# Optimization experiments

Measured on AMD Instinct MI355X. Metric: run time of the kernel, lower is better.

Reference implementation:

```python
import jax, jax.numpy as jnp
import numpy as np
from jax import lax

DN = ('NCHW', 'OIHW', 'NCHW')
NUM_HEADS = 6


def _conv1x1(x, w):
    return lax.conv_general_dilated(x, w, (1, 1), 'VALID', dimension_numbers=DN)


def _dwconv3x3(x, w):
    # depthwise 3x3, groups == channels, padding 1
    return lax.conv_general_dilated(x, w, (1, 1), ((1, 1), (1, 1)),
                                    dimension_numbers=DN,
                                    feature_group_count=w.shape[0])


def setup_inputs() -> dict:
    key = jax.random.key(0)
    ks = jax.random.split(key, 7)
    b, dim, h, w = 4, 192, 128, 128
    inp = {
        'x': jax.random.normal(ks[0], (b, dim, h, w), jnp.float32),
        'ref': jax.random.normal(ks[1], (b, dim, h, w), jnp.float32),
        'w_qkv': jax.random.normal(ks[2], (dim * 3, dim, 1, 1), jnp.float32) * 0.05,
        'w_dw': jax.random.normal(ks[3], (dim * 3, 1, 3, 3), jnp.float32) * 0.1,
        'w_proj': jax.random.normal(ks[4], (dim, dim, 1, 1), jnp.float32) * 0.05,
        'temperature': jnp.ones((NUM_HEADS, 1, 1), jnp.float32),
        'attn_w': 0.2 * jnp.ones((4,), jnp.float32),
    }
    return inp


def reference(x, ref, w_qkv, w_dw, w_proj, temperature, attn_w):
    b, c, h, w = x.shape
    heads = NUM_HEADS
    C = c // heads  # per-head channel dim
    hw = h * w

    qkv = _dwconv3x3(_conv1x1(x, w_qkv), w_dw)        # [b, 3c, h, w]
    ref_qkv = _dwconv3x3(_conv1x1(ref, w_qkv), w_dw)  # shared weights

    q_shared = qkv[:, :c]            # q from x
    k_shared = ref_qkv[:, c:2 * c]   # k from ref
    v_shared = ref_qkv[:, 2 * c:]    # v from ref

    def to_heads(t):  # [b, c, h, w] -> [b, head, C, hw]
        return t.reshape(b, heads, C, hw)

    q = to_heads(q_shared)
    k = to_heads(k_shared)
    v = to_heads(v_shared)

    # L2-normalize along token dim (last axis)
    q = q / jnp.maximum(jnp.linalg.norm(q, axis=-1, keepdims=True), 1e-12)
    k = k / jnp.maximum(jnp.linalg.norm(k, axis=-1, keepdims=True), 1e-12)

    # channel-wise attention: [b, head, C, C]
    attn = jnp.einsum('bhcn,bhdn->bhcd', q, k) * temperature

    ks_list = [int(C / 2), int(C * 2 / 3), int(C * 3 / 4), int(C * 4 / 5)]
    neg_inf = jnp.asarray(-jnp.inf, attn.dtype)

    out = 0.0
    for i, ki in enumerate(ks_list):
        vals = lax.top_k(attn, ki)[0]            # [b, head, C, ki]
        thr = vals[..., -1:]                     # k-th largest per row
        a = jnp.where(attn >= thr, attn, neg_inf)
        a = jax.nn.softmax(a, axis=-1)
        out = out + attn_w[i] * jnp.einsum('bhcd,bhdn->bhcn', a, v)

    out = out.reshape(b, c, h, w)
    return _conv1x1(out, w_proj)
```

## Files before the change

kernel.cpp:

```cpp
#include <hip/hip_runtime.h>
#include <cstdint>
#include <cstddef>

typedef unsigned short u16;
typedef unsigned int u32;
typedef __attribute__((ext_vector_type(2))) float f32x2;
typedef __attribute__((ext_vector_type(4))) float f32x4;
typedef __attribute__((ext_vector_type(8))) short short8;
typedef __attribute__((ext_vector_type(2))) u32 u32x2;
typedef __attribute__((ext_vector_type(4))) u32 u32x4;

#define DEV static __device__ __forceinline__
#define HW 16384

DEV u16 f2bf(float f) {
  u32 u = __float_as_uint(f);
  u = (u + 0x7fffu + ((u >> 16) & 1u)) >> 16;
  return (u16)u;
}
DEV float bf2f(u16 h) { return __uint_as_float(((u32)h) << 16); }

DEV u32 packsplit(float f) {
  u16 h = f2bf(f);
  u16 l = f2bf(f - bf2f(h));
  return (u32)h | ((u32)l << 16);
}
DEV void unpack8(const u32* w, short8& hi, short8& lo) {
  #pragma unroll
  for (int i = 0; i < 8; ++i) {
    hi[i] = (short)(u16)w[i];
    lo[i] = (short)(u16)(w[i] >> 16);
  }
}
DEV void mfma3(f32x4& acc, short8 ah, short8 al, short8 bh, short8 bl) {
  acc = __builtin_amdgcn_mfma_f32_16x16x32_bf16(ah, bh, acc, 0, 0, 0);
  acc = __builtin_amdgcn_mfma_f32_16x16x32_bf16(ah, bl, acc, 0, 0, 0);
  acc = __builtin_amdgcn_mfma_f32_16x16x32_bf16(al, bh, acc, 0, 0, 0);
}

__global__ __launch_bounds__(256) void ksplit(const float* __restrict__ in,
                                              u32* __restrict__ out, int n) {
  int i = blockIdx.x * 256 + threadIdx.x;
  if (i < n) out[i] = packsplit(in[i]);
}

template<int ABATCH, int BPACKED>
__global__ __launch_bounds__(512, 4) void gemm6(const u32* __restrict__ Asp,
                                                const u32* __restrict__ B0,
                                                const u32* __restrict__ B1,
                                                float* __restrict__ C0,
                                                float* __restrict__ C1) {
  __shared__ u16 Ah[192 * 32];
  __shared__ u16 Al[192 * 32];
  __shared__ u32 Bs[128 * 34];
  const int t = threadIdx.x, lane = t & 63, wid = t >> 6;
  const int b = blockIdx.z, n0 = blockIdx.x * 128, y = blockIdx.y;
  const int m0 = y * 192;
  const u32* Ab = Asp + (ABATCH ? (size_t)b * 192 * 192 : 0) + (size_t)m0 * 192;
  const u32* Bb = (y == 0 ? B0 : B1) + (size_t)b * 192 * (size_t)HW;
  float* Cb = (y == 0) ? (C0 + (size_t)b * 192 * (size_t)HW)
                       : (C1 + ((size_t)b * 384 + (size_t)(y - 1) * 192) * (size_t)HW);
  const int wr = wid >> 2, wc = wid & 3;
  const int g = lane >> 4, r16 = lane & 15;
  const int bk = t >> 4;
  const int bn = t & 15;
  f32x4 acc[6][2] = {};

  int adst[3];
  int asrc_row[3], asrc_kc[3];
  #pragma unroll
  for (int i = 0; i < 3; ++i) {
    int vi = t + i * 512;
    int row = vi >> 3, kv = (vi & 7) << 2;
    asrc_row[i] = row; asrc_kc[i] = kv;
    adst[i] = row * 32 + (((kv >> 3) ^ ((row >> 1) & 3)) << 3) + (kv & 7);
  }
  const int aswz = (g ^ ((r16 >> 1) & 3)) << 3;

  u32 Breg[8], Bnext[8];
  u32x4 Areg[3];
  #pragma unroll
  for (int j = 0; j < 8; ++j)
    Breg[j] = Bb[(size_t)bk * HW + n0 + bn + 16 * j];
  #pragma unroll
  for (int i = 0; i < 3; ++i)
    Areg[i] = *(const u32x4*)&Ab[(size_t)asrc_row[i] * 192 + asrc_kc[i]];
  #pragma unroll 1
  for (int p = 0; p < 6; ++p) {
    #pragma unroll
    for (int j = 0; j < 8; ++j)
      Bs[(bn + 16 * j) * 34 + bk] =
          BPACKED ? Breg[j] : packsplit(__uint_as_float(Breg[j]));
    #pragma unroll
    for (int i = 0; i < 3; ++i) {
      u32 h01 = (Areg[i][0] & 0xffffu) | (Areg[i][1] << 16);
      u32 h23 = (Areg[i][2] & 0xffffu) | (Areg[i][3] << 16);
      u32 l01 = (Areg[i][0] >> 16) | (Areg[i][1] & 0xffff0000u);
      u32 l23 = (Areg[i][2] >> 16) | (Areg[i][3] & 0xffff0000u);
      u32x2 hq = {h01, h23}, lq = {l01, l23};
      *(u32x2*)&Ah[adst[i]] = hq;
      *(u32x2*)&Al[adst[i]] = lq;
    }
    if (p < 5) {
      #pragma unroll
      for (int j = 0; j < 8; ++j)
        Bnext[j] = Bb[(size_t)((p + 1) * 32 + bk) * HW + n0 + bn + 16 * j];
    }
    __syncthreads();
    if (p < 5) {
      #pragma unroll
      for (int i = 0; i < 3; ++i)
        Areg[i] = *(const u32x4*)&Ab[(size_t)asrc_row[i] * 192 + (p + 1) * 32 + asrc_kc[i]];
    }
    short8 bh[2], bl[2];
    #pragma unroll
    for (int nf = 0; nf < 2; ++nf) {
      u32 bw[8];
      const u32* bp = &Bs[(wc * 32 + nf * 16 + r16) * 34 + g * 8];
      *(u32x2*)&bw[0] = *(const u32x2*)&bp[0];
      *(u32x2*)&bw[2] = *(const u32x2*)&bp[2];
      *(u32x2*)&bw[4] = *(const u32x2*)&bp[4];
      *(u32x2*)&bw[6] = *(const u32x2*)&bp[6];
      unpack8(bw, bh[nf], bl[nf]);
    }
    #pragma unroll
    for (int mf = 0; mf < 6; ++mf) {
      const int ar = (wr * 96 + mf * 16 + r16) * 32 + aswz;
      short8 ah = *(const short8*)&Ah[ar];
      short8 al = *(const short8*)&Al[ar];
      #pragma unroll
      for (int nf = 0; nf < 2; ++nf) {
        acc[mf][nf] = __builtin_amdgcn_mfma_f32_16x16x32_bf16(ah, bh[nf], acc[mf][nf], 0, 0, 0);
        acc[mf][nf] = __builtin_amdgcn_mfma_f32_16x16x32_bf16(ah, bl[nf], acc[mf][nf], 0, 0, 0);
        acc[mf][nf] = __builtin_amdgcn_mfma_f32_16x16x32_bf16(al, bh[nf], acc[mf][nf], 0, 0, 0);
      }
    }
    __syncthreads();
    #pragma unroll
    for (int j = 0; j < 8; ++j) Breg[j] = Bnext[j];
  }
  #pragma unroll
  for (int mf = 0; mf < 6; ++mf)
    #pragma unroll
    for (int nf = 0; nf < 2; ++nf)
      #pragma unroll
      for (int rr = 0; rr < 4; ++rr)
        Cb[(size_t)(wr * 96 + mf * 16 + g * 4 + rr) * HW + n0 + wc * 32 + nf * 16 + r16] =
            acc[mf][nf][rr];
}

template<int SSQ>
__global__ __launch_bounds__(512) void k2_dw(const float* __restrict__ Tin, int cstIn,
                                             const float* __restrict__ wdw, int wco,
                                             u32* __restrict__ O,
                                             float* __restrict__ ssq, int sspath) {
  const int rt = blockIdx.x, cg = blockIdx.y, b = blockIdx.z;
  const int t = threadIdx.x, lane = t & 63, w = t >> 6;
  __shared__ float In[8][10][132];
  for (int idx = t; idx < 10400; idx += 512) {
    int ch = idx / 1300, rem = idx % 1300;
    int r = rem / 130, ci = rem % 130;
    int gr = rt * 8 + r - 1, gc = ci - 1;
    float v = 0.f;
    if (gr >= 0 && gr < 128 && gc >= 0 && gc < 128)
      v = Tin[((size_t)b * cstIn + cg * 8 + ch) * HW + gr * 128 + gc];
    In[ch][r][ci] = v;
  }
  float wv[9];
  #pragma unroll
  for (int j = 0; j < 9; ++j) wv[j] = wdw[(size_t)(wco + cg * 8 + w) * 9 + j];
  __syncthreads();
  float s = 0.f;
  u32* Op = O + ((size_t)b * 192 + cg * 8 + w) * HW + rt * 8 * 128 + 2 * lane;
  #pragma unroll
  for (int i = 0; i < 8; ++i) {
    float a0 = 0.f, a1 = 0.f;
    #pragma unroll
    for (int dr = 0; dr < 3; ++dr) {
      f32x2 u0 = *(const f32x2*)&In[w][i + dr][2 * lane];
      f32x2 u1 = *(const f32x2*)&In[w][i + dr][2 * lane + 2];
      a0 += wv[dr * 3] * u0[0] + wv[dr * 3 + 1] * u0[1] + wv[dr * 3 + 2] * u1[0];
      a1 += wv[dr * 3] * u0[1] + wv[dr * 3 + 1] * u1[0] + wv[dr * 3 + 2] * u1[1];
    }
    u32x2 o = {packsplit(a0), packsplit(a1)};
    *(u32x2*)&Op[(size_t)i * 128] = o;
    if (SSQ) s += a0 * a0 + a1 * a1;
  }
  if (SSQ) {
    #pragma unroll
    for (int off = 32; off; off >>= 1) s += __shfl_down(s, off);
    if (lane == 0) ssq[(((size_t)b * 2 + sspath) * 192 + cg * 8 + w) * 16 + rt] = s;
  }
}

__global__ __launch_bounds__(256) void k3_gram(const u32* __restrict__ q,
                                               const u32* __restrict__ k,
                                               float* __restrict__ gp) {
  const int ck = blockIdx.x, bh = blockIdx.y;
  const int b = bh / 6, h = bh % 6;
  const int t = threadIdx.x, lane = t & 63, wid = t >> 6;
  const int r16 = lane & 15, g = lane >> 4;
  const int chunk = ck * 4 + wid;
  const size_t rbase = ((size_t)b * 192 + h * 32 + r16) * HW;
  const u32* qp = q + rbase;
  const u32* kp = k + rbase;
  __shared__ float red[4][1024];
  f32x4 acc[2][2] = {};
  #pragma unroll 1
  for (int s = 0; s < 8; ++s) {
    int n = chunk * 256 + s * 32 + g * 8;
    u32 wq0[8], wq1[8], wk0[8], wk1[8];
    *(u32x4*)&wq0[0] = *(const u32x4*)&qp[n];
    *(u32x4*)&wq0[4] = *(const u32x4*)&qp[n + 4];
    *(u32x4*)&wq1[0] = *(const u32x4*)&qp[(size_t)16 * HW + n];
    *(u32x4*)&wq1[4] = *(const u32x4*)&qp[(size_t)16 * HW + n + 4];
    *(u32x4*)&wk0[0] = *(const u32x4*)&kp[n];
    *(u32x4*)&wk0[4] = *(const u32x4*)&kp[n + 4];
    *(u32x4*)&wk1[0] = *(const u32x4*)&kp[(size_t)16 * HW + n];
    *(u32x4*)&wk1[4] = *(const u32x4*)&kp[(size_t)16 * HW + n + 4];
    short8 a0h, a0l, a1h, a1l, b0h, b0l, b1h, b1l;
    unpack8(wq0, a0h, a0l);
    unpack8(wq1, a1h, a1l);
    unpack8(wk0, b0h, b0l);
    unpack8(wk1, b1h, b1l);
    mfma3(acc[0][0], a0h, a0l, b0h, b0l);
    mfma3(acc[0][1], a0h, a0l, b1h, b1l);
    mfma3(acc[1][0], a1h, a1l, b0h, b0l);
    mfma3(acc[1][1], a1h, a1l, b1h, b1l);
  }
  #pragma unroll
  for (int mf = 0; mf < 2; ++mf)
    #pragma unroll
    for (int nf = 0; nf < 2; ++nf)
      #pragma unroll
      for (int rr = 0; rr < 4; ++rr)
        red[wid][(mf * 16 + g * 4 + rr) * 32 + nf * 16 + r16] = acc[mf][nf][rr];
  __syncthreads();
  float* outp = gp + ((size_t)bh * 16 + ck) * 1024;
  #pragma unroll
  for (int e = t; e < 1024; e += 256)
    outp[e] = red[0][e] + red[1][e] + red[2][e] + red[3][e];
}

__global__ __launch_bounds__(512) void k4_comb(const float* __restrict__ gp,
                                               const float* __restrict__ ssq,
                                               const float* __restrict__ temp,
                                               const float* __restrict__ aw,
                                               const float* __restrict__ wproj,
                                               u32* __restrict__ mcp) {
  const int bh = blockIdx.x, b = bh / 6, h = bh % 6;
  const int t = threadIdx.x;
  __shared__ float Gs[1024];
  __shared__ float Acm[1024];
  __shared__ float Wp[192 * 32];
  __shared__ float nq[32], nk[32];
  #pragma unroll
  for (int i = 0; i < 3; ++i) {
    int idx = t + i * 512;
    int row = idx >> 3, c4 = (idx & 7) << 2;
    *(f32x4*)&Wp[row * 32 + c4] = *(const f32x4*)&wproj[(size_t)row * 192 + h * 32 + c4];
  }
  {
    const float* p = gp + (size_t)bh * 16 * 1024 + 2 * t;
    f32x2 s = {};
    #pragma unroll
    for (int ch = 0; ch < 16; ++ch) {
      f32x2 v = *(const f32x2*)&p[(size_t)ch * 1024];
      s[0] += v[0]; s[1] += v[1];
    }
    *(f32x2*)&Gs[2 * t] = s;
  }
  if (t < 64) {
    int c = t & 31, pk = t >> 5;
    const float* sp = ssq + (((size_t)b * 2 + pk) * 192 + h * 32 + c) * 16;
    f32x4 s4 = {};
    #pragma unroll
    for (int i = 0; i < 4; ++i) {
      f32x4 v = *(const f32x4*)&sp[4 * i];
      s4[0] += v[0]; s4[1] += v[1]; s4[2] += v[2]; s4[3] += v[3];
    }
    float nr = fmaxf(sqrtf(s4[0] + s4[1] + s4[2] + s4[3]), 1e-12f);
    if (pk == 0) nq[c] = nr; else nk[c] = nr;
  }
  __syncthreads();
  const float T = temp[h];
  {
    int c = (2 * t) >> 5;
    f32x2 v = *(const f32x2*)&Gs[2 * t];
    float inq = T / nq[c];
    v[0] = v[0] * inq / nk[(2 * t) & 31];
    v[1] = v[1] * inq / nk[(2 * t + 1) & 31];
    __syncthreads();
    *(f32x2*)&Gs[2 * t] = v;
  }
  __syncthreads();
  const float aw0 = aw[0], aw1 = aw[1], aw2 = aw[2], aw3 = aw[3];
  const int half = t >> 5, d = t & 31;
  #pragma unroll
  for (int it = 0; it < 2; ++it) {
    const int c = it * 16 + half;
    const float v = Gs[c * 32 + d];
    int cnt = 0;
    #pragma unroll
    for (int dd = 0; dd < 32; ++dd) cnt += (Gs[c * 32 + dd] >= v) ? 1 : 0;
    float c0 = v;
    float c1 = (cnt >= 16) ? v : -3.0e38f;
    float c2 = (cnt >= 21) ? v : -3.0e38f;
    float c3 = (cnt >= 24) ? v : -3.0e38f;
    float c4 = (cnt >= 25) ? v : -3.0e38f;
    #pragma unroll
    for (int off = 16; off; off >>= 1) {
      c0 = fmaxf(c0, __shfl_xor(c0, off));
      c1 = fmaxf(c1, __shfl_xor(c1, off));
      c2 = fmaxf(c2, __shfl_xor(c2, off));
      c3 = fmaxf(c3, __shfl_xor(c3, off));
      c4 = fmaxf(c4, __shfl_xor(c4, off));
    }
    const float m = c0;
    const float ex = expf(v - m);
    float z1 = (v >= c1) ? ex : 0.f;
    float z2 = (v >= c2) ? ex : 0.f;
    float z3 = (v >= c3) ? ex : 0.f;
    float z4 = (v >= c4) ? ex : 0.f;
    #pragma unroll
    for (int off = 16; off; off >>= 1) {
      z1 += __shfl_xor(z1, off);
      z2 += __shfl_xor(z2, off);
      z3 += __shfl_xor(z3, off);
      z4 += __shfl_xor(z4, off);
    }
    float a = 0.f;
    a += (v >= c1) ? aw0 * ex / z1 : 0.f;
    a += (v >= c2) ? aw1 * ex / z2 : 0.f;
    a += (v >= c3) ? aw2 * ex / z3 : 0.f;
    a += (v >= c4) ? aw3 * ex / z4 : 0.f;
    Acm[c * 32 + d] = a;
  }
  __syncthreads();
  #pragma unroll
  for (int i = 0; i < 12; ++i) {
    int idx = t + i * 512;
    int co = idx >> 5, dd = idx & 31;
    float s = 0.f;
    #pragma unroll
    for (int c = 0; c < 32; ++c) s += Wp[co * 32 + c] * Acm[c * 32 + dd];
    mcp[((size_t)b * 192 + co) * 192 + h * 32 + dd] = packsplit(s);
  }
}

extern "C" void kernel_launch(void* const* d_in, const int* in_sizes, int n_in,
                              void* d_out, int out_size, void* d_ws, size_t ws_size,
                              hipStream_t stream) {
  const float* x     = (const float*)d_in[0];
  const float* ref   = (const float*)d_in[1];
  const float* wqkv  = (const float*)d_in[2];
  const float* wdw   = (const float*)d_in[3];
  const float* wproj = (const float*)d_in[4];
  const float* temp  = (const float*)d_in[5];
  const float* aw    = (const float*)d_in[6];
  float* out = (float*)d_out;
  char* ws = (char*)d_ws;

  const size_t S = (size_t)4 * 192 * HW * 4;
  float* Ckv = (float*)(ws);
  float* Cq  = (float*)(ws + 2 * S);
  u32*   qpk = (u32*)(ws + 3 * S);
  float* gp  = (float*)(ws + 4 * S);
  float* ssq = (float*)(ws + 4 * S + 1572864);
  u32*   wsp = (u32*)(ws + 4 * S + 1572864 + 98304);
  u32*   mcp = (u32*)(ws + 4 * S + 1572864 + 98304 + 442368);
  u32*   kpk = (u32*)Cq;
  u32*   vpk = qpk;

  ksplit<<<dim3(432), 256, 0, stream>>>(wqkv, wsp, 576 * 192);
  gemm6<0, 0><<<dim3(128, 3, 4), 512, 0, stream>>>(wsp, (const u32*)x, (const u32*)ref,
                                                   Cq, Ckv);
  k2_dw<1><<<dim3(16, 24, 4), 512, 0, stream>>>(Cq, 192, wdw, 0, qpk, ssq, 0);
  k2_dw<1><<<dim3(16, 24, 4), 512, 0, stream>>>(Ckv, 384, wdw, 192, kpk, ssq, 1);
  k3_gram<<<dim3(16, 24), 256, 0, stream>>>(qpk, kpk, gp);
  k2_dw<0><<<dim3(16, 24, 4), 512, 0, stream>>>(Ckv + (size_t)192 * HW, 384, wdw, 384,
                                                vpk, nullptr, 2);
  k4_comb<<<dim3(24), 512, 0, stream>>>(gp, ssq, temp, aw, wproj, mcp);
  gemm6<1, 1><<<dim3(128, 1, 4), 512, 0, stream>>>(mcp, vpk, vpk, out, out);
}
```

Baseline: 208.2 us.

## Pre-swizzle split A operand into MFMA fragment layout and load directly from global

The weight-split kernel and the combine kernel now write the hi/lo bf16 halves of the A matrices in a layout matching the MFMA per-lane fragment order. The GEMM then reads A fragments straight from global (L2-cached) memory with one short8 load per lane, dropping the A shared-memory staging, its repacking and its LDS bank traffic. This cuts LDS usage and per-iteration instructions, at the cost of A loads from global/L2 inside the inner loop with less latency hiding.

```diff
diff --git a/kernel.cpp b/kernel.cpp
--- a/kernel.cpp
+++ b/kernel.cpp
@@ -38,25 +38,32 @@
   acc = __builtin_amdgcn_mfma_f32_16x16x32_bf16(al, bh, acc, 0, 0, 0);
 }
 
-__global__ __launch_bounds__(256) void ksplit(const float* __restrict__ in,
-                                              u32* __restrict__ out, int n) {
+
+__global__ __launch_bounds__(256) void ksplit2(const float* __restrict__ in,
+                                               u16* __restrict__ oh,
+                                               u16* __restrict__ ol, int n) {
   int i = blockIdx.x * 256 + threadIdx.x;
-  if (i < n) out[i] = packsplit(in[i]);
+  if (i >= n) return;
+  int R = i / 192, K = i % 192;
+  int halfblk = R / 96, rem = R % 96, mf = rem >> 4, r = rem & 15;
+  int p = K >> 5, kk = K & 31, g = kk >> 3, j = kk & 7;
+  size_t o16 = (((size_t)halfblk * 6 + p) * 6 + mf) * 512 + (size_t)(g * 16 + r) * 8 + j;
+  float f = in[i];
+  u16 h = f2bf(f);
+  oh[o16] = h;
+  ol[o16] = f2bf(f - bf2f(h));
 }
 
 template<int ABATCH, int BPACKED>
-__global__ __launch_bounds__(512, 4) void gemm6(const u32* __restrict__ Asp,
+__global__ __launch_bounds__(512, 4) void gemm7(const u16* __restrict__ Afh,
+                                                const u16* __restrict__ Afl,
                                                 const u32* __restrict__ B0,
                                                 const u32* __restrict__ B1,
                                                 float* __restrict__ C0,
                                                 float* __restrict__ C1) {
-  __shared__ u16 Ah[192 * 32];
-  __shared__ u16 Al[192 * 32];
   __shared__ u32 Bs[128 * 34];
   const int t = threadIdx.x, lane = t & 63, wid = t >> 6;
   const int b = blockIdx.z, n0 = blockIdx.x * 128, y = blockIdx.y;
-  const int m0 = y * 192;
-  const u32* Ab = Asp + (ABATCH ? (size_t)b * 192 * 192 : 0) + (size_t)m0 * 192;
   const u32* Bb = (y == 0 ? B0 : B1) + (size_t)b * 192 * (size_t)HW;
   float* Cb = (y == 0) ? (C0 + (size_t)b * 192 * (size_t)HW)
                        : (C1 + ((size_t)b * 384 + (size_t)(y - 1) * 192) * (size_t)HW);
@@ -64,54 +71,27 @@
   const int g = lane >> 4, r16 = lane & 15;
   const int bk = t >> 4;
   const int bn = t & 15;
+  const int halfblk = (ABATCH ? b : y) * 2 + wr;
+  const u16* Ah_w = Afh + (size_t)halfblk * 36 * 512 + (size_t)lane * 8;
+  const u16* Al_w = Afl + (size_t)halfblk * 36 * 512 + (size_t)lane * 8;
   f32x4 acc[6][2] = {};
 
-  int adst[3];
-  int asrc_row[3], asrc_kc[3];
-  #pragma unroll
-  for (int i = 0; i < 3; ++i) {
-    int vi = t + i * 512;
-    int row = vi >> 3, kv = (vi & 7) << 2;
-    asrc_row[i] = row; asrc_kc[i] = kv;
-    adst[i] = row * 32 + (((kv >> 3) ^ ((row >> 1) & 3)) << 3) + (kv & 7);
-  }
-  const int aswz = (g ^ ((r16 >> 1) & 3)) << 3;
-
   u32 Breg[8], Bnext[8];
-  u32x4 Areg[3];
   #pragma unroll
   for (int j = 0; j < 8; ++j)
     Breg[j] = Bb[(size_t)bk * HW + n0 + bn + 16 * j];
-  #pragma unroll
-  for (int i = 0; i < 3; ++i)
-    Areg[i] = *(const u32x4*)&Ab[(size_t)asrc_row[i] * 192 + asrc_kc[i]];
   #pragma unroll 1
   for (int p = 0; p < 6; ++p) {
     #pragma unroll
     for (int j = 0; j < 8; ++j)
       Bs[(bn + 16 * j) * 34 + bk] =
           BPACKED ? Breg[j] : packsplit(__uint_as_float(Breg[j]));
-    #pragma unroll
-    for (int i = 0; i < 3; ++i) {
-      u32 h01 = (Areg[i][0] & 0xffffu) | (Areg[i][1] << 16);
-      u32 h23 = (Areg[i][2] & 0xffffu) | (Areg[i][3] << 16);
-      u32 l01 = (Areg[i][0] >> 16) | (Areg[i][1] & 0xffff0000u);
-      u32 l23 = (Areg[i][2] >> 16) | (Areg[i][3] & 0xffff0000u);
-      u32x2 hq = {h01, h23}, lq = {l01, l23};
-      *(u32x2*)&Ah[adst[i]] = hq;
-      *(u32x2*)&Al[adst[i]] = lq;
-    }
     if (p < 5) {
       #pragma unroll
       for (int j = 0; j < 8; ++j)
         Bnext[j] = Bb[(size_t)((p + 1) * 32 + bk) * HW + n0 + bn + 16 * j];
     }
     __syncthreads();
-    if (p < 5) {
-      #pragma unroll
-      for (int i = 0; i < 3; ++i)
-        Areg[i] = *(const u32x4*)&Ab[(size_t)asrc_row[i] * 192 + (p + 1) * 32 + asrc_kc[i]];
-    }
     short8 bh[2], bl[2];
     #pragma unroll
     for (int nf = 0; nf < 2; ++nf) {
@@ -125,9 +105,9 @@
     }
     #pragma unroll
     for (int mf = 0; mf < 6; ++mf) {
-      const int ar = (wr * 96 + mf * 16 + r16) * 32 + aswz;
-      short8 ah = *(const short8*)&Ah[ar];
-      short8 al = *(const short8*)&Al[ar];
+      const int fo = (p * 6 + mf) << 9;
+      short8 ah = *(const short8*)(Ah_w + fo);
+      short8 al = *(const short8*)(Al_w + fo);
       #pragma unroll
       for (int nf = 0; nf < 2; ++nf) {
         acc[mf][nf] = __builtin_amdgcn_mfma_f32_16x16x32_bf16(ah, bh[nf], acc[mf][nf], 0, 0, 0);
@@ -247,7 +227,8 @@
                                                const float* __restrict__ temp,
                                                const float* __restrict__ aw,
                                                const float* __restrict__ wproj,
-                                               u32* __restrict__ mcp) {
+                                               u16* __restrict__ mfh,
+                                               u16* __restrict__ mfl) {
   const int bh = blockIdx.x, b = bh / 6, h = bh % 6;
   const int t = threadIdx.x;
   __shared__ float Gs[1024];
@@ -344,7 +325,12 @@
     float s = 0.f;
     #pragma unroll
     for (int c = 0; c < 32; ++c) s += Wp[co * 32 + c] * Acm[c * 32 + dd];
-    mcp[((size_t)b * 192 + co) * 192 + h * 32 + dd] = packsplit(s);
+    int wr2 = co / 96, rem = co % 96, mf = rem >> 4, r = rem & 15;
+    int lane2 = ((dd >> 3) << 4) + r, j = dd & 7;
+    size_t o16 = ((((size_t)b * 2 + wr2) * 6 + h) * 6 + mf) * 512 + (size_t)lane2 * 8 + j;
+    u16 hh = f2bf(s);
+    mfh[o16] = hh;
+    mfl[o16] = f2bf(s - bf2f(hh));
   }
 }
 
@@ -365,21 +351,24 @@
   float* Ckv = (float*)(ws);
   float* Cq  = (float*)(ws + 2 * S);
   u32*   qpk = (u32*)(ws + 3 * S);
-  float* gp  = (float*)(ws + 4 * S);
-  float* ssq = (float*)(ws + 4 * S + 1572864);
-  u32*   wsp = (u32*)(ws + 4 * S + 1572864 + 98304);
-  u32*   mcp = (u32*)(ws + 4 * S + 1572864 + 98304 + 442368);
+  char*  p5  = ws + 4 * S;
+  float* gp  = (float*)(p5);
+  float* ssq = (float*)(p5 + 1572864);
+  u16*   afh = (u16*)(p5 + 1572864 + 98304);
+  u16*   afl = (u16*)(p5 + 1572864 + 98304 + 221184);
+  u16*   mfh = (u16*)(p5 + 1572864 + 98304 + 2 * 221184);
+  u16*   mfl = (u16*)(p5 + 1572864 + 98304 + 2 * 221184 + 294912);
   u32*   kpk = (u32*)Cq;
   u32*   vpk = qpk;
 
-  ksplit<<<dim3(432), 256, 0, stream>>>(wqkv, wsp, 576 * 192);
-  gemm6<0, 0><<<dim3(128, 3, 4), 512, 0, stream>>>(wsp, (const u32*)x, (const u32*)ref,
-                                                   Cq, Ckv);
+  ksplit2<<<dim3(432), 256, 0, stream>>>(wqkv, afh, afl, 576 * 192);
+  gemm7<0, 0><<<dim3(128, 3, 4), 512, 0, stream>>>(afh, afl, (const u32*)x,
+                                                   (const u32*)ref, Cq, Ckv);
   k2_dw<1><<<dim3(16, 24, 4), 512, 0, stream>>>(Cq, 192, wdw, 0, qpk, ssq, 0);
   k2_dw<1><<<dim3(16, 24, 4), 512, 0, stream>>>(Ckv, 384, wdw, 192, kpk, ssq, 1);
   k3_gram<<<dim3(16, 24), 256, 0, stream>>>(qpk, kpk, gp);
   k2_dw<0><<<dim3(16, 24, 4), 512, 0, stream>>>(Ckv + (size_t)192 * HW, 384, wdw, 384,
                                                 vpk, nullptr, 2);
-  k4_comb<<<dim3(24), 512, 0, stream>>>(gp, ssq, temp, aw, wproj, mcp);
-  gemm6<1, 1><<<dim3(128, 1, 4), 512, 0, stream>>>(mcp, vpk, vpk, out, out);
-}
+  k4_comb<<<dim3(24), 512, 0, stream>>>(gp, ssq, temp, aw, wproj, mfh, mfl);
+  gemm7<1, 1><<<dim3(128, 1, 4), 512, 0, stream>>>(mfh, mfl, vpk, vpk, out, out);
+}
```

Measured after the change: 215.9 us. 3.7% more time.
